# Performance work log

Hardware: AMD Instinct MI355X
Metric: run time of the kernel (lower is better)

Reference implementation:

```python
import jax, jax.numpy as jnp
import numpy as np

B, T, D_IN, H = 128, 256, 512, 1024

def setup_inputs() -> dict:
    key = jax.random.key(0)
    ks = jax.random.split(key, 12)
    s = 1.0 / np.sqrt(H)
    return {
        "input": jax.random.normal(ks[0], (B, T, D_IN), jnp.float32),
        "h0": jax.random.normal(ks[1], (B, H), jnp.float32),
        "c0": jax.random.normal(ks[2], (B, H), jnp.float32),
        "ctx": jax.random.normal(ks[3], (B, T, H), jnp.float32),
        "srcmask": jax.random.randint(ks[4], (B, T), 0, 2).astype(bool),
        "W_ih": jax.random.uniform(ks[5], (4 * H, D_IN), jnp.float32, -s, s),
        "W_hh": jax.random.uniform(ks[6], (4 * H, H), jnp.float32, -s, s),
        "b_ih": jax.random.uniform(ks[7], (4 * H,), jnp.float32, -s, s),
        "b_hh": jax.random.uniform(ks[8], (4 * H,), jnp.float32, -s, s),
        "W_attn": jax.random.uniform(ks[9], (H, H), jnp.float32, -s, s),
        "W_out": jax.random.uniform(ks[10], (H, 2 * H), jnp.float32, -s, s),
    }


def reference(input, h0, c0, ctx, srcmask, W_ih, W_hh, b_ih, b_hh, W_attn, W_out):
    def step(carry, x_t):
        h, c = carry
        # LSTMCell: gate order i, f, g, o (PyTorch convention)
        gates = x_t @ W_ih.T + b_ih + h @ W_hh.T + b_hh  # [B, 4H]
        i_g, f_g, g_g, o_g = jnp.split(gates, 4, axis=-1)
        cy = jax.nn.sigmoid(f_g) * c + jax.nn.sigmoid(i_g) * jnp.tanh(g_g)
        hy = jax.nn.sigmoid(o_g) * jnp.tanh(cy)
        # Bilinear attention: score(K_j, q) = K_j^T (W_attn q)
        q = hy @ W_attn.T                                   # [B, H]
        scores = jnp.einsum("blh,bh->bl", ctx, q)          # [B, L]
        scores = jnp.where(srcmask, -jnp.inf, scores)
        probs = jax.nn.softmax(scores, axis=-1)
        wctx = jnp.einsum("bl,blh->bh", probs, ctx)        # [B, H]
        h_tilde = jnp.tanh(jnp.concatenate([wctx, hy], axis=-1) @ W_out.T)
        return (h_tilde, cy), h_tilde

    xs = jnp.transpose(input, (1, 0, 2))  # [T, B, D_IN]
    (h_f, c_f), outs = jax.lax.scan(step, (h0, c0), xs)
    output = jnp.transpose(outs, (1, 0, 2))  # [B, T, H]
    return (output, h_f, c_f)
```

## Files before the change

### kernel.cpp

```cpp
#include <hip/hip_runtime.h>
#include <hip/hip_bf16.h>
#include <math.h>

#define B_  128
#define T_  256
#define DIN 512
#define H_  1024

typedef __attribute__((ext_vector_type(8))) short bf16x8;
typedef __attribute__((ext_vector_type(4))) float f32x4;

#define GLD_LDS16(gsrc, ldst) \
  __builtin_amdgcn_global_load_lds((const __attribute__((address_space(1))) void*)(gsrc), \
                                   (__attribute__((address_space(3))) void*)(ldst), 16, 0, 0)

__device__ __forceinline__ void split_bf16(float v, __hip_bfloat16* hi, __hip_bfloat16* lo) {
    __hip_bfloat16 h = __float2bfloat16(v);
    *hi = h;
    *lo = __float2bfloat16(v - __bfloat162float(h));
}

template<int N> __device__ __forceinline__ void waitvm() {
    if constexpr (N == 0)       asm volatile("s_waitcnt vmcnt(0)" ::: "memory");
    else if constexpr (N == 10) asm volatile("s_waitcnt vmcnt(10)" ::: "memory");
    else static_assert(N == 0 || N == 10, "add vmcnt literal");
}

__global__ void bias_sum_k(const float* __restrict__ a, const float* __restrict__ b,
                           float* __restrict__ o, int n) {
    int i = blockIdx.x * blockDim.x + threadIdx.x;
    if (i < n) o[i] = a[i] + b[i];
}

__global__ void detect_mask_k(const int* __restrict__ m, int nwords, int* __restrict__ flag) {
    __shared__ int bad;
    if (threadIdx.x == 0) bad = 0;
    __syncthreads();
    for (int i = threadIdx.x; i < nwords; i += blockDim.x) {
        unsigned v = (unsigned)m[i];
        if (v > 1u) bad = 1;
    }
    __syncthreads();
    if (threadIdx.x == 0) flag[0] = bad ? 0 : 1;
}

__global__ void cvt_split_k(const float* __restrict__ s, __hip_bfloat16* __restrict__ hi,
                            __hip_bfloat16* __restrict__ lo, int n) {
    int i = blockIdx.x * 256 + threadIdx.x;
    if (i < n) split_bf16(s[i], hi + i, lo + i);
}

__global__ void wg_split_k(const float* __restrict__ Wih, const float* __restrict__ Whh,
                           __hip_bfloat16* __restrict__ Wh, __hip_bfloat16* __restrict__ Wl) {
    int i = blockIdx.x * 256 + threadIdx.x;
    int n = i / 1536, c = i - n * 1536;
    float v = (c < DIN) ? Wih[n * DIN + c] : Whh[n * H_ + (c - DIN)];
    split_bf16(v, Wh + i, Wl + i);
}

__device__ __forceinline__ void cvtx_body(int i, const float* __restrict__ xsrc,
                                          __hip_bfloat16* __restrict__ xh,
                                          __hip_bfloat16* __restrict__ xl) {
    int b = i >> 9, c = i & 511;
    split_bf16(xsrc[(size_t)b * (T_ * DIN) + c], xh + i, xl + i);
}

__global__ void cvtx_k(const float* __restrict__ xsrc, __hip_bfloat16* __restrict__ xh,
                       __hip_bfloat16* __restrict__ xl) {
    cvtx_body(blockIdx.x * 256 + threadIdx.x, xsrc, xh, xl);
}

template<int NT>
__global__ __launch_bounds__(256)
void mfma_gemm_k(const __hip_bfloat16* __restrict__ A1h, const __hip_bfloat16* __restrict__ A1l,
                 long lda1, int K1,
                 const __hip_bfloat16* __restrict__ A2h, const __hip_bfloat16* __restrict__ A2l,
                 long lda2,
                 const __hip_bfloat16* __restrict__ Wh, const __hip_bfloat16* __restrict__ Wl,
                 long ldw,
                 float* __restrict__ Cpart, long ldc, long pstride)
{
    constexpr int APL = 128 * 64 * 2;
    constexpr int BPL = 32 * 64 * 2;
    constexpr int BUFB = 2 * APL + 2 * BPL;
    __shared__ __attribute__((aligned(16))) char lds[3 * BUFB];

    const int tid = threadIdx.x;
    const int l = tid & 63, w = tid >> 6;
    const int n0 = blockIdx.x * 32;
    const int kbase = blockIdx.y * (NT * 64);
    const int wm = (w >> 1) * 64, wn = (w & 1) * 16;

    auto stage = [&](int buf, int kt) {
        char* base = lds + buf * BUFB;
        const int kb = kbase + kt * 64;
        #pragma unroll
        for (int p = 0; p < 2; ++p) {
            const __hip_bfloat16* A1 = p ? A1l : A1h;
            const __hip_bfloat16* A2 = p ? A2l : A2h;
            #pragma unroll
            for (int j = 0; j < 4; ++j) {
                int c = j * 256 + tid;
                int row = c >> 3, slot = c & 7;
                int e = kb + ((slot ^ (row & 7)) << 3);
                const __hip_bfloat16* src = (e < K1) ? (A1 + (long)row * lda1 + e)
                                                     : (A2 + (long)row * lda2 + (e - K1));
                GLD_LDS16(src, base + p * APL + ((j * 256 + (tid & 192)) << 4));
            }
            {
                int row = tid >> 3, slot = tid & 7;
                int e = kb + ((slot ^ (row & 7)) << 3);
                const __hip_bfloat16* src = (p ? Wl : Wh) + (long)(n0 + row) * ldw + e;
                GLD_LDS16(src, base + 2 * APL + p * BPL + ((tid & 192) << 4));
            }
        }
    };

    f32x4 acc[4] = {};

    stage(0, 0);
    if (NT > 1) stage(1, 1);

    for (int kt = 0; kt < NT; ++kt) {
        if (kt + 1 < NT) waitvm<10>(); else waitvm<0>();
        __builtin_amdgcn_s_barrier();
        __builtin_amdgcn_sched_barrier(0);
        if (kt + 2 < NT) stage((kt + 2) % 3, kt + 2);

        const char* base = lds + (kt % 3) * BUFB;
        #pragma unroll
        for (int ks = 0; ks < 2; ++ks) {
            bf16x8 afh[4], afl[4], bh, bl;
            #pragma unroll
            for (int mi = 0; mi < 4; ++mi) {
                int row = wm + mi * 16 + (l & 15);
                int slot = (l >> 4) + ks * 4;
                int off = row * 128 + ((slot ^ (row & 7)) << 4);
                afh[mi] = *(const bf16x8*)(base + off);
                afl[mi] = *(const bf16x8*)(base + APL + off);
            }
            {
                int row = wn + (l & 15);
                int slot = (l >> 4) + ks * 4;
                int off = row * 128 + ((slot ^ (row & 7)) << 4);
                bh = *(const bf16x8*)(base + 2 * APL + off);
                bl = *(const bf16x8*)(base + 2 * APL + BPL + off);
            }
            #pragma unroll
            for (int mi = 0; mi < 4; ++mi) {
                acc[mi] = __builtin_amdgcn_mfma_f32_16x16x32_bf16(afh[mi], bh, acc[mi], 0, 0, 0);
                acc[mi] = __builtin_amdgcn_mfma_f32_16x16x32_bf16(afl[mi], bh, acc[mi], 0, 0, 0);
                acc[mi] = __builtin_amdgcn_mfma_f32_16x16x32_bf16(afh[mi], bl, acc[mi], 0, 0, 0);
            }
        }
    }

    float* Cb = Cpart + (long)blockIdx.y * pstride;
    const int n = n0 + wn + (l & 15);
    #pragma unroll
    for (int mi = 0; mi < 4; ++mi) {
        int mbase = wm + mi * 16 + (l >> 4) * 4;
        #pragma unroll
        for (int r = 0; r < 4; ++r)
            Cb[(long)(mbase + r) * ldc + n] = acc[mi][r];
    }
}

__device__ __forceinline__ float sigmoidf_(float x) { return 1.f / (1.f + expf(-x)); }

__global__ __launch_bounds__(256)
void cell_cvtx_k(const float* __restrict__ gpart,
                 const float* __restrict__ bsum,
                 const float* __restrict__ cprev, float* __restrict__ cy,
                 __hip_bfloat16* __restrict__ AoBh, __hip_bfloat16* __restrict__ AoBl,
                 float* __restrict__ cf,
                 const float* __restrict__ xnext,
                 __hip_bfloat16* __restrict__ xh, __hip_bfloat16* __restrict__ xl)
{
    int bid = blockIdx.x;
    if (bid < 512) {
        int idx = bid * 256 + threadIdx.x;
        int b = idx >> 10, j = idx & 1023;
        const float* g0 = gpart + ((size_t)b << 12);
        const float* g1 = g0 + (size_t)128 * 4096;
        float ig = sigmoidf_(g0[j]        + g1[j]        + bsum[j]);
        float fg = sigmoidf_(g0[1024 + j] + g1[1024 + j] + bsum[1024 + j]);
        float gg = tanhf    (g0[2048 + j] + g1[2048 + j] + bsum[2048 + j]);
        float og = sigmoidf_(g0[3072 + j] + g1[3072 + j] + bsum[3072 + j]);
        float c = fg * cprev[idx] + ig * gg;
        float h = og * tanhf(c);
        cy[idx] = c;
        split_bf16(h, AoBh + (size_t)b * 2048 + 1024 + j, AoBl + (size_t)b * 2048 + 1024 + j);
        if (cf) cf[idx] = c;
    } else if (xnext) {
        cvtx_body((bid - 512) * 256 + threadIdx.x, xnext, xh, xl);
    }
}

__global__ __launch_bounds__(256)
void attn_k(const float* __restrict__ ctx, const float* __restrict__ qpart,
            const void* __restrict__ maskp, const int* __restrict__ mflag,
            __hip_bfloat16* __restrict__ AoBh, __hip_bfloat16* __restrict__ AoBl)
{
    constexpr int L = T_, H = H_;
    int b = blockIdx.x;
    const float* cb = ctx + (size_t)b * L * H;
    int tid = threadIdx.x, l = tid & 63, w = tid >> 6;
    int mode = mflag[0];

    float rq[16];
    #pragma unroll
    for (int j = 0; j < 16; ++j) {
        size_t o = (size_t)b * H + l + j * 64;
        rq[j] = qpart[o] + qpart[o + 131072] + qpart[o + 262144] + qpart[o + 393216];
    }

    float m = -INFINITY, s = 0.f, acc[16] = {};
    for (int li = w; li < L; li += 4) {
        bool msk = mode ? (((const int*)maskp)[b * L + li] != 0)
                        : (((const unsigned char*)maskp)[b * L + li] != 0);
        if (msk) continue;
        const float* cr = cb + (size_t)li * H;
        float rc[16], d = 0.f;
        #pragma unroll
        for (int j = 0; j < 16; ++j) { rc[j] = cr[l + j * 64]; d += rc[j] * rq[j]; }
        #pragma unroll
        for (int off = 1; off < 64; off <<= 1) d += __shfl_xor(d, off);
        float mn = fmaxf(m, d);
        float f = expf(m - mn);
        float p = expf(d - mn);
        s = s * f + p;
        #pragma unroll
        for (int j = 0; j < 16; ++j) acc[j] = acc[j] * f + p * rc[j];
        m = mn;
    }

    __shared__ float sacc[4][H_];
    __shared__ float sms[4][2];
    #pragma unroll
    for (int j = 0; j < 16; ++j) sacc[w][l + j * 64] = acc[j];
    if (l == 0) { sms[w][0] = m; sms[w][1] = s; }
    __syncthreads();

    float M = fmaxf(fmaxf(sms[0][0], sms[1][0]), fmaxf(sms[2][0], sms[3][0]));
    float fw[4], S = 0.f;
    #pragma unroll
    for (int ww = 0; ww < 4; ++ww) { fw[ww] = expf(sms[ww][0] - M); S += fw[ww] * sms[ww][1]; }
    float inv = 1.f / S;
    for (int k = tid; k < H; k += 256) {
        float a = sacc[0][k] * fw[0] + sacc[1][k] * fw[1] + sacc[2][k] * fw[2] + sacc[3][k] * fw[3];
        split_bf16(a * inv, AoBh + (size_t)b * 2048 + k, AoBl + (size_t)b * 2048 + k);
    }
}

__global__ __launch_bounds__(256)
void outred_k(const float* __restrict__ opart,
              __hip_bfloat16* __restrict__ hth, __hip_bfloat16* __restrict__ htl,
              float* __restrict__ outp,
              float* __restrict__ hf)
{
    int idx = blockIdx.x * 256 + threadIdx.x;
    int b = idx >> 10, j = idx & 1023;
    float v = opart[idx] + opart[idx + 131072] + opart[idx + 262144] + opart[idx + 393216];
    v = tanhf(v);
    split_bf16(v, hth + idx, htl + idx);
    outp[(size_t)b * (T_ * H_) + j] = v;
    if (hf) hf[idx] = v;
}

extern "C" void kernel_launch(void* const* d_in, const int* in_sizes, int n_in,
                              void* d_out, int out_size, void* d_ws, size_t ws_size,
                              hipStream_t stream)
{
    const float* input  = (const float*)d_in[0];
    const float* h0     = (const float*)d_in[1];
    const float* c0     = (const float*)d_in[2];
    const float* ctx    = (const float*)d_in[3];
    const void*  srcmask= d_in[4];
    const float* W_ih   = (const float*)d_in[5];
    const float* W_hh   = (const float*)d_in[6];
    const float* b_ih   = (const float*)d_in[7];
    const float* b_hh   = (const float*)d_in[8];
    const float* W_attn = (const float*)d_in[9];
    const float* W_out  = (const float*)d_in[10];

    constexpr int B = B_, T = T_, D = DIN, H = H_;

    float* f = (float*)d_ws;
    float* bsum  = f; f += 4 * H;
    float* cbuf  = f; f += (size_t)B * H;
    float* gpart = f; f += (size_t)2 * B * 4 * H;
    float* qpart = f; f += (size_t)4 * B * H;
    float* opart = f; f += (size_t)4 * B * H;
    int*   mflag = (int*)f; f += 64;
    __hip_bfloat16* p = (__hip_bfloat16*)f;
    __hip_bfloat16* Wgh = p; p += (size_t)4 * H * (D + H);
    __hip_bfloat16* Wgl = p; p += (size_t)4 * H * (D + H);
    __hip_bfloat16* Wah = p; p += (size_t)H * H;
    __hip_bfloat16* Wal = p; p += (size_t)H * H;
    __hip_bfloat16* Woh = p; p += (size_t)H * 2 * H;
    __hip_bfloat16* Wol = p; p += (size_t)H * 2 * H;
    __hip_bfloat16* hth = p; p += (size_t)B * H;
    __hip_bfloat16* htl = p; p += (size_t)B * H;
    __hip_bfloat16* AoBh = p; p += (size_t)B * 2 * H;
    __hip_bfloat16* AoBl = p; p += (size_t)B * 2 * H;
    __hip_bfloat16* xth[2], *xtl[2];
    xth[0] = p; p += (size_t)B * D;
    xtl[0] = p; p += (size_t)B * D;
    xth[1] = p; p += (size_t)B * D;
    xtl[1] = p; p += (size_t)B * D;

    float* out = (float*)d_out;
    float* hf  = out + (size_t)B * T * H;
    float* cf  = hf + (size_t)B * H;

    hipMemcpyAsync(cbuf, c0, (size_t)B * H * sizeof(float), hipMemcpyDeviceToDevice, stream);
    bias_sum_k<<<dim3(16), dim3(256), 0, stream>>>(b_ih, b_hh, bsum, 4 * H);
    detect_mask_k<<<dim3(1), dim3(256), 0, stream>>>((const int*)srcmask, B * T / 4, mflag);
    wg_split_k<<<dim3(4 * H * (D + H) / 256), dim3(256), 0, stream>>>(W_ih, W_hh, Wgh, Wgl);
    cvt_split_k<<<dim3(H * H / 256), dim3(256), 0, stream>>>(W_attn, Wah, Wal, H * H);
    cvt_split_k<<<dim3(H * 2 * H / 256), dim3(256), 0, stream>>>(W_out, Woh, Wol, H * 2 * H);
    cvt_split_k<<<dim3(B * H / 256), dim3(256), 0, stream>>>(h0, hth, htl, B * H);
    cvtx_k<<<dim3(B * D / 256), dim3(256), 0, stream>>>(input, xth[0], xtl[0]);

    dim3 blk(256);
    for (int t = 0; t < T; ++t) {
        int sl = t & 1, sn = sl ^ 1;

        mfma_gemm_k<12><<<dim3(128, 2), blk, 0, stream>>>(
            xth[sl], xtl[sl], D, D,
            hth, htl, H,
            Wgh, Wgl, D + H,
            gpart, 4 * H, (long)B * 4 * H);

        cell_cvtx_k<<<dim3(768), blk, 0, stream>>>(
            gpart, bsum, cbuf, cbuf, AoBh, AoBl, (t == T - 1) ? cf : nullptr,
            (t + 1 < T) ? input + (size_t)(t + 1) * D : nullptr, xth[sn], xtl[sn]);

        mfma_gemm_k<4><<<dim3(32, 4), blk, 0, stream>>>(
            AoBh + H, AoBl + H, 2 * H, 2 * H,
            AoBh + H, AoBl + H, 2 * H,
            Wah, Wal, H,
            qpart, H, (long)B * H);

        attn_k<<<dim3(B), blk, 0, stream>>>(ctx, qpart, srcmask, mflag, AoBh, AoBl);

        mfma_gemm_k<8><<<dim3(32, 4), blk, 0, stream>>>(
            AoBh, AoBl, 2 * H, 2 * H,
            AoBh, AoBl, 2 * H,
            Woh, Wol, 2 * H,
            opart, H, (long)B * H);

        outred_k<<<dim3(512), blk, 0, stream>>>(
            opart, hth, htl, out + (size_t)t * H, (t == T - 1) ? hf : nullptr);
    }
}
```

Measured before the change: 18.29 ms.

## Fuse per-timestep kernels into one persistent kernel with grid barriers

Replaces the six kernel launches per timestep (over 1500 launches in total) with a single persistent kernel of 256 blocks. The blocks synchronise between phases through atomic-counter grid barriers. The attention and output GEMMs now use an 8-way K split so all 256 blocks have work, and attention is split into two halves per batch row, merged with a log-sum-exp combine phase. The aim is to remove launch overhead and idle gaps between small kernels. In exchange it adds seven grid barriers per step and relies on all 256 blocks being co-resident.

```diff
diff --git a/kernel.cpp b/kernel.cpp
--- a/kernel.cpp
+++ b/kernel.cpp
@@ -20,11 +20,7 @@
     *lo = __float2bfloat16(v - __bfloat162float(h));
 }
 
-template<int N> __device__ __forceinline__ void waitvm() {
-    if constexpr (N == 0)       asm volatile("s_waitcnt vmcnt(0)" ::: "memory");
-    else if constexpr (N == 10) asm volatile("s_waitcnt vmcnt(10)" ::: "memory");
-    else static_assert(N == 0 || N == 10, "add vmcnt literal");
-}
+__device__ __forceinline__ float sigmoidf_(float x) { return 1.f / (1.f + expf(-x)); }
 
 __global__ void bias_sum_k(const float* __restrict__ a, const float* __restrict__ b,
                            float* __restrict__ o, int n) {
@@ -70,202 +66,259 @@
     cvtx_body(blockIdx.x * 256 + threadIdx.x, xsrc, xh, xl);
 }
 
-template<int NT>
-__global__ __launch_bounds__(256)
-void mfma_gemm_k(const __hip_bfloat16* __restrict__ A1h, const __hip_bfloat16* __restrict__ A1l,
-                 long lda1, int K1,
-                 const __hip_bfloat16* __restrict__ A2h, const __hip_bfloat16* __restrict__ A2l,
-                 long lda2,
-                 const __hip_bfloat16* __restrict__ Wh, const __hip_bfloat16* __restrict__ Wl,
-                 long ldw,
-                 float* __restrict__ Cpart, long ldc, long pstride)
+constexpr int APL = 128 * 64 * 2;
+constexpr int BPL = 32 * 64 * 2;
+constexpr int BUFB = 2 * APL + 2 * BPL;
+constexpr int LDSZ = 3 * BUFB;
+
+struct P {
+    const float* input; const float* ctx; const void* srcmask;
+    const float* bsum; float* cbuf;
+    float* gpart; float* qpart; float* opart;
+    float* pacc; float* pm; float* ps;
+    const int* mflag; unsigned* cnt;
+    const __hip_bfloat16 *Wgh, *Wgl, *Wah, *Wal, *Woh, *Wol;
+    __hip_bfloat16 *hth, *htl, *AoBh, *AoBl;
+    __hip_bfloat16 *xth0, *xtl0, *xth1, *xtl1;
+    float* out; float* hf; float* cf;
+};
+
+#define GBAR() do { \
+    __syncthreads(); \
+    if (tid == 0) { \
+        __threadfence(); \
+        __hip_atomic_fetch_add(&p.cnt[slot], 1u, __ATOMIC_RELAXED, __HIP_MEMORY_SCOPE_AGENT); \
+        while (__hip_atomic_load(&p.cnt[slot], __ATOMIC_RELAXED, __HIP_MEMORY_SCOPE_AGENT) < 256u) \
+            __builtin_amdgcn_s_sleep(8); \
+        __threadfence(); \
+    } \
+    ++slot; \
+    __syncthreads(); \
+  } while (0)
+
+#define GEMM_PHASE(NT, NB, KSP, A1H, A1L, LDA1, K1V, A2H, A2L, LDA2, WHP, WLP, LDW, CP, LDC, PSTRIDE) \
+  { \
+    const int n0_ = (NB) * 32; \
+    const int kbase_ = (KSP) * ((NT) * 64); \
+    const int wm_ = (w >> 1) * 64, wn_ = (w & 1) * 16; \
+    auto stage = [&](int buf, int kt) { \
+        char* base = lds + buf * BUFB; \
+        const int kb = kbase_ + kt * 64; \
+        _Pragma("unroll") \
+        for (int pp = 0; pp < 2; ++pp) { \
+            const __hip_bfloat16* A1 = pp ? (A1L) : (A1H); \
+            const __hip_bfloat16* A2 = pp ? (A2L) : (A2H); \
+            _Pragma("unroll") \
+            for (int j = 0; j < 4; ++j) { \
+                int c = j * 256 + tid; \
+                int row = c >> 3, sl2 = c & 7; \
+                int e = kb + ((sl2 ^ (row & 7)) << 3); \
+                const __hip_bfloat16* src = (e < (K1V)) ? (A1 + (long)row * (LDA1) + e) \
+                                                        : (A2 + (long)row * (LDA2) + (e - (K1V))); \
+                GLD_LDS16(src, base + pp * APL + ((j * 256 + (tid & 192)) << 4)); \
+            } \
+            { \
+                int row = tid >> 3, sl2 = tid & 7; \
+                int e = kb + ((sl2 ^ (row & 7)) << 3); \
+                const __hip_bfloat16* src = (pp ? (WLP) : (WHP)) + (long)(n0_ + row) * (LDW) + e; \
+                GLD_LDS16(src, base + 2 * APL + pp * BPL + ((tid & 192) << 4)); \
+            } \
+        } \
+    }; \
+    f32x4 acc[4] = {}; \
+    stage(0, 0); \
+    if ((NT) > 1) stage(1, 1); \
+    for (int kt = 0; kt < (NT); ++kt) { \
+        if (kt + 1 < (NT)) asm volatile("s_waitcnt vmcnt(10)" ::: "memory"); \
+        else               asm volatile("s_waitcnt vmcnt(0)"  ::: "memory"); \
+        __builtin_amdgcn_s_barrier(); \
+        __builtin_amdgcn_sched_barrier(0); \
+        if (kt + 2 < (NT)) stage((kt + 2) % 3, kt + 2); \
+        const char* base = lds + (kt % 3) * BUFB; \
+        _Pragma("unroll") \
+        for (int ks = 0; ks < 2; ++ks) { \
+            bf16x8 afh[4], afl[4], bh, bl; \
+            _Pragma("unroll") \
+            for (int mi = 0; mi < 4; ++mi) { \
+                int row = wm_ + mi * 16 + (l & 15); \
+                int sl2 = (l >> 4) + ks * 4; \
+                int off = row * 128 + ((sl2 ^ (row & 7)) << 4); \
+                afh[mi] = *(const bf16x8*)(base + off); \
+                afl[mi] = *(const bf16x8*)(base + APL + off); \
+            } \
+            { \
+                int row = wn_ + (l & 15); \
+                int sl2 = (l >> 4) + ks * 4; \
+                int off = row * 128 + ((sl2 ^ (row & 7)) << 4); \
+                bh = *(const bf16x8*)(base + 2 * APL + off); \
+                bl = *(const bf16x8*)(base + 2 * APL + BPL + off); \
+            } \
+            _Pragma("unroll") \
+            for (int mi = 0; mi < 4; ++mi) { \
+                acc[mi] = __builtin_amdgcn_mfma_f32_16x16x32_bf16(afh[mi], bh, acc[mi], 0, 0, 0); \
+                acc[mi] = __builtin_amdgcn_mfma_f32_16x16x32_bf16(afl[mi], bh, acc[mi], 0, 0, 0); \
+                acc[mi] = __builtin_amdgcn_mfma_f32_16x16x32_bf16(afh[mi], bl, acc[mi], 0, 0, 0); \
+            } \
+        } \
+    } \
+    float* Cb = (CP) + (long)(KSP) * (PSTRIDE); \
+    const int n = n0_ + wn_ + (l & 15); \
+    _Pragma("unroll") \
+    for (int mi = 0; mi < 4; ++mi) { \
+        int mbase = wm_ + mi * 16 + (l >> 4) * 4; \
+        _Pragma("unroll") \
+        for (int r = 0; r < 4; ++r) \
+            Cb[(long)(mbase + r) * (LDC) + n] = acc[mi][r]; \
+    } \
+  }
+
+__global__ __launch_bounds__(256, 1)
+void fused_k(P p)
 {
-    constexpr int APL = 128 * 64 * 2;
-    constexpr int BPL = 32 * 64 * 2;
-    constexpr int BUFB = 2 * APL + 2 * BPL;
-    __shared__ __attribute__((aligned(16))) char lds[3 * BUFB];
-
+    __shared__ __attribute__((aligned(16))) char lds[LDSZ];
+    const int blk = blockIdx.x;
     const int tid = threadIdx.x;
     const int l = tid & 63, w = tid >> 6;
-    const int n0 = blockIdx.x * 32;
-    const int kbase = blockIdx.y * (NT * 64);
-    const int wm = (w >> 1) * 64, wn = (w & 1) * 16;
-
-    auto stage = [&](int buf, int kt) {
-        char* base = lds + buf * BUFB;
-        const int kb = kbase + kt * 64;
+    unsigned slot = 0;
+
+    for (int t = 0; t < T_; ++t) {
+        const __hip_bfloat16* xh = (t & 1) ? p.xth1 : p.xth0;
+        const __hip_bfloat16* xl = (t & 1) ? p.xtl1 : p.xtl0;
+
+        GEMM_PHASE(12, (blk & 127), (blk >> 7),
+                   xh, xl, DIN, DIN,
+                   p.hth, p.htl, H_,
+                   p.Wgh, p.Wgl, (DIN + H_),
+                   p.gpart, (4 * H_), ((long)B_ * 4 * H_));
+        GBAR();
+
         #pragma unroll
-        for (int p = 0; p < 2; ++p) {
-            const __hip_bfloat16* A1 = p ? A1l : A1h;
-            const __hip_bfloat16* A2 = p ? A2l : A2h;
+        for (int i = 0; i < 2; ++i) {
+            int idx = blk * 512 + i * 256 + tid;
+            int b = idx >> 10, j = idx & 1023;
+            const float* g0 = p.gpart + ((size_t)b << 12) + j;
+            const float* g1 = g0 + (size_t)B_ * 4 * H_;
+            float ig = sigmoidf_(g0[0]    + g1[0]    + p.bsum[j]);
+            float fg = sigmoidf_(g0[1024] + g1[1024] + p.bsum[1024 + j]);
+            float gg = tanhf    (g0[2048] + g1[2048] + p.bsum[2048 + j]);
+            float og = sigmoidf_(g0[3072] + g1[3072] + p.bsum[3072 + j]);
+            float c = fg * p.cbuf[idx] + ig * gg;
+            float h = og * tanhf(c);
+            p.cbuf[idx] = c;
+            split_bf16(h, p.AoBh + (size_t)b * 2048 + 1024 + j,
+                          p.AoBl + (size_t)b * 2048 + 1024 + j);
+            if (t == T_ - 1) p.cf[idx] = c;
+        }
+        if (t + 1 < T_) {
+            __hip_bfloat16* nxh = (t & 1) ? p.xth0 : p.xth1;
+            __hip_bfloat16* nxl = (t & 1) ? p.xtl0 : p.xtl1;
+            cvtx_body(blk * 256 + tid, p.input + (size_t)(t + 1) * DIN, nxh, nxl);
+        }
+        GBAR();
+
+        GEMM_PHASE(2, (blk & 31), (blk >> 5),
+                   (p.AoBh + H_), (p.AoBl + H_), (2 * H_), (2 * H_),
+                   (p.AoBh + H_), (p.AoBl + H_), (2 * H_),
+                   p.Wah, p.Wal, H_,
+                   p.qpart, H_, ((long)B_ * H_));
+        GBAR();
+
+        {
+            const int b = blk >> 1, half = blk & 1;
+            const float* cb = p.ctx + (size_t)b * (T_ * H_);
+            const int mode = p.mflag[0];
+
+            float rq[16];
             #pragma unroll
-            for (int j = 0; j < 4; ++j) {
-                int c = j * 256 + tid;
-                int row = c >> 3, slot = c & 7;
-                int e = kb + ((slot ^ (row & 7)) << 3);
-                const __hip_bfloat16* src = (e < K1) ? (A1 + (long)row * lda1 + e)
-                                                     : (A2 + (long)row * lda2 + (e - K1));
-                GLD_LDS16(src, base + p * APL + ((j * 256 + (tid & 192)) << 4));
+            for (int j = 0; j < 16; ++j) {
+                size_t o = (size_t)b * H_ + l + j * 64;
+                float s = 0.f;
+                #pragma unroll
+                for (int ss = 0; ss < 8; ++ss) s += p.qpart[o + (size_t)ss * (B_ * H_)];
+                rq[j] = s;
             }
-            {
-                int row = tid >> 3, slot = tid & 7;
-                int e = kb + ((slot ^ (row & 7)) << 3);
-                const __hip_bfloat16* src = (p ? Wl : Wh) + (long)(n0 + row) * ldw + e;
-                GLD_LDS16(src, base + 2 * APL + p * BPL + ((tid & 192) << 4));
+
+            float m = -INFINITY, s = 0.f, acc[16] = {};
+            const int base = half * 128;
+            for (int li = base + w; li < base + 128; li += 4) {
+                bool msk = mode ? (((const int*)p.srcmask)[b * T_ + li] != 0)
+                                : (((const unsigned char*)p.srcmask)[b * T_ + li] != 0);
+                if (msk) continue;
+                const float* cr = cb + (size_t)li * H_;
+                float rc[16], d = 0.f;
+                #pragma unroll
+                for (int j = 0; j < 16; ++j) { rc[j] = cr[l + j * 64]; d += rc[j] * rq[j]; }
+                #pragma unroll
+                for (int off = 1; off < 64; off <<= 1) d += __shfl_xor(d, off);
+                float mn = fmaxf(m, d);
+                float f = expf(m - mn);
+                float pp = expf(d - mn);
+                s = s * f + pp;
+                #pragma unroll
+                for (int j = 0; j < 16; ++j) acc[j] = acc[j] * f + pp * rc[j];
+                m = mn;
             }
-        }
-    };
-
-    f32x4 acc[4] = {};
-
-    stage(0, 0);
-    if (NT > 1) stage(1, 1);
-
-    for (int kt = 0; kt < NT; ++kt) {
-        if (kt + 1 < NT) waitvm<10>(); else waitvm<0>();
-        __builtin_amdgcn_s_barrier();
-        __builtin_amdgcn_sched_barrier(0);
-        if (kt + 2 < NT) stage((kt + 2) % 3, kt + 2);
-
-        const char* base = lds + (kt % 3) * BUFB;
+
+            float (*sacc)[H_] = (float (*)[H_])lds;
+            float (*sms)[2]   = (float (*)[2])(lds + 4 * H_ * sizeof(float));
+            __syncthreads();
+            #pragma unroll
+            for (int j = 0; j < 16; ++j) sacc[w][l + j * 64] = acc[j];
+            if (l == 0) { sms[w][0] = m; sms[w][1] = s; }
+            __syncthreads();
+
+            float M = fmaxf(fmaxf(sms[0][0], sms[1][0]), fmaxf(sms[2][0], sms[3][0]));
+            float fw[4], S = 0.f;
+            #pragma unroll
+            for (int ww = 0; ww < 4; ++ww) {
+                fw[ww] = (sms[ww][0] == -INFINITY) ? 0.f : expf(sms[ww][0] - M);
+                S += fw[ww] * sms[ww][1];
+            }
+            int ph = b * 2 + half;
+            for (int k = tid; k < H_; k += 256) {
+                float a = sacc[0][k] * fw[0] + sacc[1][k] * fw[1] + sacc[2][k] * fw[2] + sacc[3][k] * fw[3];
+                p.pacc[(size_t)ph * H_ + k] = a;
+            }
+            if (tid == 0) { p.pm[ph] = M; p.ps[ph] = S; }
+        }
+        GBAR();
+
         #pragma unroll
-        for (int ks = 0; ks < 2; ++ks) {
-            bf16x8 afh[4], afl[4], bh, bl;
+        for (int i = 0; i < 2; ++i) {
+            int idx = blk * 512 + i * 256 + tid;
+            int b = idx >> 10, k = idx & 1023;
+            float m0 = p.pm[2 * b], m1 = p.pm[2 * b + 1];
+            float M = fmaxf(m0, m1);
+            float f0 = (m0 == -INFINITY) ? 0.f : expf(m0 - M);
+            float f1 = (m1 == -INFINITY) ? 0.f : expf(m1 - M);
+            float S = f0 * p.ps[2 * b] + f1 * p.ps[2 * b + 1];
+            float v = (p.pacc[(size_t)(2 * b) * H_ + k] * f0 +
+                       p.pacc[(size_t)(2 * b + 1) * H_ + k] * f1) / S;
+            split_bf16(v, p.AoBh + (size_t)b * 2048 + k, p.AoBl + (size_t)b * 2048 + k);
+        }
+        GBAR();
+
+        GEMM_PHASE(4, (blk & 31), (blk >> 5),
+                   p.AoBh, p.AoBl, (2 * H_), (2 * H_),
+                   p.AoBh, p.AoBl, (2 * H_),
+                   p.Woh, p.Wol, (2 * H_),
+                   p.opart, H_, ((long)B_ * H_));
+        GBAR();
+
+        #pragma unroll
+        for (int i = 0; i < 2; ++i) {
+            int idx = blk * 512 + i * 256 + tid;
+            int b = idx >> 10, j = idx & 1023;
+            float v = 0.f;
             #pragma unroll
-            for (int mi = 0; mi < 4; ++mi) {
-                int row = wm + mi * 16 + (l & 15);
-                int slot = (l >> 4) + ks * 4;
-                int off = row * 128 + ((slot ^ (row & 7)) << 4);
-                afh[mi] = *(const bf16x8*)(base + off);
-                afl[mi] = *(const bf16x8*)(base + APL + off);
-            }
-            {
-                int row = wn + (l & 15);
-                int slot = (l >> 4) + ks * 4;
-                int off = row * 128 + ((slot ^ (row & 7)) << 4);
-                bh = *(const bf16x8*)(base + 2 * APL + off);
-                bl = *(const bf16x8*)(base + 2 * APL + BPL + off);
-            }
-            #pragma unroll
-            for (int mi = 0; mi < 4; ++mi) {
-                acc[mi] = __builtin_amdgcn_mfma_f32_16x16x32_bf16(afh[mi], bh, acc[mi], 0, 0, 0);
-                acc[mi] = __builtin_amdgcn_mfma_f32_16x16x32_bf16(afl[mi], bh, acc[mi], 0, 0, 0);
-                acc[mi] = __builtin_amdgcn_mfma_f32_16x16x32_bf16(afh[mi], bl, acc[mi], 0, 0, 0);
-            }
-        }
+            for (int ss = 0; ss < 8; ++ss) v += p.opart[idx + ss * (B_ * H_)];
+            v = tanhf(v);
+            split_bf16(v, p.hth + idx, p.htl + idx);
+            p.out[(size_t)b * (T_ * H_) + (size_t)t * H_ + j] = v;
+            if (t == T_ - 1) p.hf[idx] = v;
+        }
+        GBAR();
     }
-
-    float* Cb = Cpart + (long)blockIdx.y * pstride;
-    const int n = n0 + wn + (l & 15);
-    #pragma unroll
-    for (int mi = 0; mi < 4; ++mi) {
-        int mbase = wm + mi * 16 + (l >> 4) * 4;
-        #pragma unroll
-        for (int r = 0; r < 4; ++r)
-            Cb[(long)(mbase + r) * ldc + n] = acc[mi][r];
-    }
-}
-
-__device__ __forceinline__ float sigmoidf_(float x) { return 1.f / (1.f + expf(-x)); }
-
-__global__ __launch_bounds__(256)
-void cell_cvtx_k(const float* __restrict__ gpart,
-                 const float* __restrict__ bsum,
-                 const float* __restrict__ cprev, float* __restrict__ cy,
-                 __hip_bfloat16* __restrict__ AoBh, __hip_bfloat16* __restrict__ AoBl,
-                 float* __restrict__ cf,
-                 const float* __restrict__ xnext,
-                 __hip_bfloat16* __restrict__ xh, __hip_bfloat16* __restrict__ xl)
-{
-    int bid = blockIdx.x;
-    if (bid < 512) {
-        int idx = bid * 256 + threadIdx.x;
-        int b = idx >> 10, j = idx & 1023;
-        const float* g0 = gpart + ((size_t)b << 12);
-        const float* g1 = g0 + (size_t)128 * 4096;
-        float ig = sigmoidf_(g0[j]        + g1[j]        + bsum[j]);
-        float fg = sigmoidf_(g0[1024 + j] + g1[1024 + j] + bsum[1024 + j]);
-        float gg = tanhf    (g0[2048 + j] + g1[2048 + j] + bsum[2048 + j]);
-        float og = sigmoidf_(g0[3072 + j] + g1[3072 + j] + bsum[3072 + j]);
-        float c = fg * cprev[idx] + ig * gg;
-        float h = og * tanhf(c);
-        cy[idx] = c;
-        split_bf16(h, AoBh + (size_t)b * 2048 + 1024 + j, AoBl + (size_t)b * 2048 + 1024 + j);
-        if (cf) cf[idx] = c;
-    } else if (xnext) {
-        cvtx_body((bid - 512) * 256 + threadIdx.x, xnext, xh, xl);
-    }
-}
-
-__global__ __launch_bounds__(256)
-void attn_k(const float* __restrict__ ctx, const float* __restrict__ qpart,
-            const void* __restrict__ maskp, const int* __restrict__ mflag,
-            __hip_bfloat16* __restrict__ AoBh, __hip_bfloat16* __restrict__ AoBl)
-{
-    constexpr int L = T_, H = H_;
-    int b = blockIdx.x;
-    const float* cb = ctx + (size_t)b * L * H;
-    int tid = threadIdx.x, l = tid & 63, w = tid >> 6;
-    int mode = mflag[0];
-
-    float rq[16];
-    #pragma unroll
-    for (int j = 0; j < 16; ++j) {
-        size_t o = (size_t)b * H + l + j * 64;
-        rq[j] = qpart[o] + qpart[o + 131072] + qpart[o + 262144] + qpart[o + 393216];
-    }
-
-    float m = -INFINITY, s = 0.f, acc[16] = {};
-    for (int li = w; li < L; li += 4) {
-        bool msk = mode ? (((const int*)maskp)[b * L + li] != 0)
-                        : (((const unsigned char*)maskp)[b * L + li] != 0);
-        if (msk) continue;
-        const float* cr = cb + (size_t)li * H;
-        float rc[16], d = 0.f;
-        #pragma unroll
-        for (int j = 0; j < 16; ++j) { rc[j] = cr[l + j * 64]; d += rc[j] * rq[j]; }
-        #pragma unroll
-        for (int off = 1; off < 64; off <<= 1) d += __shfl_xor(d, off);
-        float mn = fmaxf(m, d);
-        float f = expf(m - mn);
-        float p = expf(d - mn);
-        s = s * f + p;
-        #pragma unroll
-        for (int j = 0; j < 16; ++j) acc[j] = acc[j] * f + p * rc[j];
-        m = mn;
-    }
-
-    __shared__ float sacc[4][H_];
-    __shared__ float sms[4][2];
-    #pragma unroll
-    for (int j = 0; j < 16; ++j) sacc[w][l + j * 64] = acc[j];
-    if (l == 0) { sms[w][0] = m; sms[w][1] = s; }
-    __syncthreads();
-
-    float M = fmaxf(fmaxf(sms[0][0], sms[1][0]), fmaxf(sms[2][0], sms[3][0]));
-    float fw[4], S = 0.f;
-    #pragma unroll
-    for (int ww = 0; ww < 4; ++ww) { fw[ww] = expf(sms[ww][0] - M); S += fw[ww] * sms[ww][1]; }
-    float inv = 1.f / S;
-    for (int k = tid; k < H; k += 256) {
-        float a = sacc[0][k] * fw[0] + sacc[1][k] * fw[1] + sacc[2][k] * fw[2] + sacc[3][k] * fw[3];
-        split_bf16(a * inv, AoBh + (size_t)b * 2048 + k, AoBl + (size_t)b * 2048 + k);
-    }
-}
-
-__global__ __launch_bounds__(256)
-void outred_k(const float* __restrict__ opart,
-              __hip_bfloat16* __restrict__ hth, __hip_bfloat16* __restrict__ htl,
-              float* __restrict__ outp,
-              float* __restrict__ hf)
-{
-    int idx = blockIdx.x * 256 + threadIdx.x;
-    int b = idx >> 10, j = idx & 1023;
-    float v = opart[idx] + opart[idx + 131072] + opart[idx + 262144] + opart[idx + 393216];
-    v = tanhf(v);
-    split_bf16(v, hth + idx, htl + idx);
-    outp[(size_t)b * (T_ * H_) + j] = v;
-    if (hf) hf[idx] = v;
 }
 
 extern "C" void kernel_launch(void* const* d_in, const int* in_sizes, int n_in,
@@ -290,9 +343,13 @@
     float* bsum  = f; f += 4 * H;
     float* cbuf  = f; f += (size_t)B * H;
     float* gpart = f; f += (size_t)2 * B * 4 * H;
-    float* qpart = f; f += (size_t)4 * B * H;
-    float* opart = f; f += (size_t)4 * B * H;
+    float* qpart = f; f += (size_t)8 * B * H;
+    float* opart = f; f += (size_t)8 * B * H;
+    float* pacc  = f; f += (size_t)2 * B * H;
+    float* pm    = f; f += 256;
+    float* ps    = f; f += 256;
     int*   mflag = (int*)f; f += 64;
+    unsigned* cnt = (unsigned*)f; f += 2048;
     __hip_bfloat16* p = (__hip_bfloat16*)f;
     __hip_bfloat16* Wgh = p; p += (size_t)4 * H * (D + H);
     __hip_bfloat16* Wgl = p; p += (size_t)4 * H * (D + H);
@@ -304,16 +361,16 @@
     __hip_bfloat16* htl = p; p += (size_t)B * H;
     __hip_bfloat16* AoBh = p; p += (size_t)B * 2 * H;
     __hip_bfloat16* AoBl = p; p += (size_t)B * 2 * H;
-    __hip_bfloat16* xth[2], *xtl[2];
-    xth[0] = p; p += (size_t)B * D;
-    xtl[0] = p; p += (size_t)B * D;
-    xth[1] = p; p += (size_t)B * D;
-    xtl[1] = p; p += (size_t)B * D;
+    __hip_bfloat16* xth0 = p; p += (size_t)B * D;
+    __hip_bfloat16* xtl0 = p; p += (size_t)B * D;
+    __hip_bfloat16* xth1 = p; p += (size_t)B * D;
+    __hip_bfloat16* xtl1 = p; p += (size_t)B * D;
 
     float* out = (float*)d_out;
     float* hf  = out + (size_t)B * T * H;
     float* cf  = hf + (size_t)B * H;
 
+    hipMemsetAsync(cnt, 0, 2048 * sizeof(unsigned), stream);
     hipMemcpyAsync(cbuf, c0, (size_t)B * H * sizeof(float), hipMemcpyDeviceToDevice, stream);
     bias_sum_k<<<dim3(16), dim3(256), 0, stream>>>(b_ih, b_hh, bsum, 4 * H);
     detect_mask_k<<<dim3(1), dim3(256), 0, stream>>>((const int*)srcmask, B * T / 4, mflag);
@@ -321,37 +378,19 @@
     cvt_split_k<<<dim3(H * H / 256), dim3(256), 0, stream>>>(W_attn, Wah, Wal, H * H);
     cvt_split_k<<<dim3(H * 2 * H / 256), dim3(256), 0, stream>>>(W_out, Woh, Wol, H * 2 * H);
     cvt_split_k<<<dim3(B * H / 256), dim3(256), 0, stream>>>(h0, hth, htl, B * H);
-    cvtx_k<<<dim3(B * D / 256), dim3(256), 0, stream>>>(input, xth[0], xtl[0]);
-
-    dim3 blk(256);
-    for (int t = 0; t < T; ++t) {
-        int sl = t & 1, sn = sl ^ 1;
-
-        mfma_gemm_k<12><<<dim3(128, 2), blk, 0, stream>>>(
-            xth[sl], xtl[sl], D, D,
-            hth, htl, H,
-            Wgh, Wgl, D + H,
-            gpart, 4 * H, (long)B * 4 * H);
-
-        cell_cvtx_k<<<dim3(768), blk, 0, stream>>>(
-            gpart, bsum, cbuf, cbuf, AoBh, AoBl, (t == T - 1) ? cf : nullptr,
-            (t + 1 < T) ? input + (size_t)(t + 1) * D : nullptr, xth[sn], xtl[sn]);
-
-        mfma_gemm_k<4><<<dim3(32, 4), blk, 0, stream>>>(
-            AoBh + H, AoBl + H, 2 * H, 2 * H,
-            AoBh + H, AoBl + H, 2 * H,
-            Wah, Wal, H,
-            qpart, H, (long)B * H);
-
-        attn_k<<<dim3(B), blk, 0, stream>>>(ctx, qpart, srcmask, mflag, AoBh, AoBl);
-
-        mfma_gemm_k<8><<<dim3(32, 4), blk, 0, stream>>>(
-            AoBh, AoBl, 2 * H, 2 * H,
-            AoBh, AoBl, 2 * H,
-            Woh, Wol, 2 * H,
-            opart, H, (long)B * H);
-
-        outred_k<<<dim3(512), blk, 0, stream>>>(
-            opart, hth, htl, out + (size_t)t * H, (t == T - 1) ? hf : nullptr);
-    }
-}
+    cvtx_k<<<dim3(B * D / 256), dim3(256), 0, stream>>>(input, xth0, xtl0);
+
+    P prm;
+    prm.input = input; prm.ctx = ctx; prm.srcmask = srcmask;
+    prm.bsum = bsum; prm.cbuf = cbuf;
+    prm.gpart = gpart; prm.qpart = qpart; prm.opart = opart;
+    prm.pacc = pacc; prm.pm = pm; prm.ps = ps;
+    prm.mflag = mflag; prm.cnt = cnt;
+    prm.Wgh = Wgh; prm.Wgl = Wgl; prm.Wah = Wah; prm.Wal = Wal;
+    prm.Woh = Woh; prm.Wol = Wol;
+    prm.hth = hth; prm.htl = htl; prm.AoBh = AoBh; prm.AoBl = AoBl;
+    prm.xth0 = xth0; prm.xtl0 = xtl0; prm.xth1 = xth1; prm.xtl1 = xtl1;
+    prm.out = out; prm.hf = hf; prm.cf = cf;
+
+    fused_k<<<dim3(256), dim3(256), 0, stream>>>(prm);
+}
```

Measured after the change: 71.79 ms. +292.4%, slower.
